# Optimization experiments

Measured on AMD Instinct MI355X. Metric: run time of the kernel, lower is better.

## Reference

```python
import jax, jax.numpy as jnp
import numpy as np

B, S, H, E, V = 64, 512, 1024, 512, 32000
D = 2  # bidirectional encoder -> memory dim = D*H


def setup_inputs() -> dict:
    key = jax.random.key(0)
    ks = jax.random.split(key, 16)
    sc = lambda n: 1.0 / np.sqrt(n)
    return {
        "word": jax.random.randint(ks[0], (B,), 1, V),
        "hidden": jax.random.normal(ks[1], (B, H), jnp.float32),
        "encoder_outputs": jax.random.normal(ks[2], (B, S, D * H), jnp.float32),
        "output_distribution": jax.random.uniform(ks[3], (B, V), jnp.float32),
        "encoder_attention": jax.random.uniform(ks[4], (B, S), jnp.float32),
        # embedding (padding_idx=0 row zeroed)
        "emb": jax.random.normal(ks[5], (V, E), jnp.float32).at[0].set(0.0) * 0.02,
        # Bah_Attn params
        "lin1_w": jax.random.normal(ks[6], (H, H), jnp.float32) * sc(H),
        "lin1_b": jnp.zeros((H,), jnp.float32),
        "lin2_w": jax.random.normal(ks[7], (H, D * H), jnp.float32) * sc(D * H),
        "lin2_b": jnp.zeros((H,), jnp.float32),
        "v_w": jax.random.normal(ks[8], (1, H), jnp.float32) * sc(H),
        "v_b": jnp.zeros((1,), jnp.float32),
        # GRUCell params: input = context(2H) + word_vec(E) = 2560
        "W_ih": jax.random.normal(ks[9], (3 * H, D * H + E), jnp.float32) * sc(H),
        "b_ih": jnp.zeros((3 * H,), jnp.float32),
        "W_hh": jax.random.normal(ks[10], (3 * H, H), jnp.float32) * sc(H),
        "b_hh": jnp.zeros((3 * H,), jnp.float32),
        # output projection
        "out_w": jax.random.normal(ks[11], (V, H), jnp.float32) * sc(H),
        "out_b": jnp.zeros((V,), jnp.float32),
    }


def reference(word, hidden, encoder_outputs, output_distribution, encoder_attention,
              emb, lin1_w, lin1_b, lin2_w, lin2_b, v_w, v_b,
              W_ih, b_ih, W_hh, b_hh, out_w, out_b):
    # word embedding lookup (feed_word_emb='word')
    word_vec = emb[word]                                   # [B, E]
    h_x = hidden @ lin1_w.T + lin1_b                       # [B, H]
    h_m = jnp.einsum('bsm,hm->bsh', encoder_outputs, lin2_w) + lin2_b  # [B, S, H]
    e = jnp.tanh(h_x[:, None, :] + h_m) @ v_w[0] + v_b[0]  # [B, S]
    score = jax.nn.softmax(e, axis=-1)                     # [B, S]
    context = jnp.einsum('bs,bsm->bm', score, encoder_outputs)  # [B, 2H]
    # GRUCell step on cat([context, word_vec])
    x = jnp.concatenate([context, word_vec], axis=1)       # [B, 2H+E]
    gi = x @ W_ih.T + b_ih                                 # [B, 3H]
    gh = hidden @ W_hh.T + b_hh                            # [B, 3H]
    i_r, i_z, i_n = jnp.split(gi, 3, axis=1)
    h_r, h_z, h_n = jnp.split(gh, 3, axis=1)
    r = jax.nn.sigmoid(i_r + h_r)
    z = jax.nn.sigmoid(i_z + h_z)
    n = jnp.tanh(i_n + r * h_n)
    new_hidden = (1.0 - z) * n + z * hidden                # [B, H]
    pred_word = new_hidden @ out_w.T + out_b               # [B, V]
    return (pred_word, new_hidden, score)
```

## Files before the change

kernel.cpp:

```cpp
#include <hip/hip_runtime.h>
#include <hip/hip_bf16.h>
#include <stdint.h>

typedef __attribute__((ext_vector_type(4))) float f32x4;
typedef __attribute__((ext_vector_type(8))) short short8;

#define B_   64
#define S_   512
#define H_   1024
#define E_   512
#define V_   32000
#define M_   2048
#define BS_  32768
#define XIN_ 2560
#define G3_  3072

__device__ __forceinline__ unsigned short f2bf(float f) {
  union { float f; unsigned u; } x; x.f = f;
  unsigned r = x.u + 0x7fffu + ((x.u >> 16) & 1u);
  return (unsigned short)(r >> 16);
}

__device__ __forceinline__ float bf2f(unsigned short u) {
  union { unsigned u; float f; } x; x.u = (unsigned)u << 16; return x.f;
}

__device__ __forceinline__ void async16(const void* g, void* l) {
  __builtin_amdgcn_global_load_lds((const __attribute__((address_space(1))) unsigned*)g,
                                   (__attribute__((address_space(3))) unsigned*)l,
                                   16, 0, 0);
}

__global__ __launch_bounds__(256) void k_conv(const float* __restrict__ enc,
                                              unsigned short* __restrict__ ebf,
                                              const float* __restrict__ lin2w,
                                              unsigned short* __restrict__ bw,
                                              const int* __restrict__ word,
                                              const float* __restrict__ emb,
                                              float* __restrict__ wv) {
  const size_t NENC8 = (size_t)BS_ * M_ / 8;
  const size_t NW8   = (size_t)H_ * M_ / 8;
  const size_t NWV4  = (size_t)B_ * E_ / 4;
  const size_t total = NENC8 + NW8 + NWV4;
  for (size_t idx = (size_t)blockIdx.x * 256 + threadIdx.x; idx < total;
       idx += (size_t)gridDim.x * 256) {
    if (idx < NENC8) {
      f32x4 a = *(const f32x4*)(enc + idx * 8);
      f32x4 b = *(const f32x4*)(enc + idx * 8 + 4);
      short8 o = { (short)f2bf(a.x), (short)f2bf(a.y), (short)f2bf(a.z), (short)f2bf(a.w),
                   (short)f2bf(b.x), (short)f2bf(b.y), (short)f2bf(b.z), (short)f2bf(b.w) };
      *(short8*)(ebf + idx * 8) = o;
    } else if (idx < NENC8 + NW8) {
      size_t i = idx - NENC8;
      f32x4 a = *(const f32x4*)(lin2w + i * 8);
      f32x4 b = *(const f32x4*)(lin2w + i * 8 + 4);
      short8 o = { (short)f2bf(a.x), (short)f2bf(a.y), (short)f2bf(a.z), (short)f2bf(a.w),
                   (short)f2bf(b.x), (short)f2bf(b.y), (short)f2bf(b.z), (short)f2bf(b.w) };
      *(short8*)(bw + i * 8) = o;
    } else {
      size_t i = idx - NENC8 - NW8;
      int i0 = (int)i * 4;
      int b = i0 >> 9, c = i0 & 511;
      f32x4 v = *(const f32x4*)(emb + (size_t)word[b] * E_ + c);
      *(f32x4*)(wv + i0) = v;
    }
  }
}

__global__ __launch_bounds__(256) void k_hx(const float* __restrict__ hidden,
                                            const float* __restrict__ w1,
                                            const float* __restrict__ b1,
                                            const float* __restrict__ b2,
                                            float* __restrict__ hx) {
  __shared__ float hs[64][36];
  __shared__ float Ws[64][36];
  const int t = threadIdx.x;
  const int hbase = blockIdx.x * 64;
  const int hb = t & 15, bb = t >> 4;
  const int srow = t >> 2, sc0 = (t & 3) * 8;
  float acc[4][4] = {};
  for (int kc = 0; kc < H_; kc += 32) {
    *(f32x4*)&hs[srow][sc0]     = *(const f32x4*)(hidden + (size_t)srow * H_ + kc + sc0);
    *(f32x4*)&hs[srow][sc0 + 4] = *(const f32x4*)(hidden + (size_t)srow * H_ + kc + sc0 + 4);
    *(f32x4*)&Ws[srow][sc0]     = *(const f32x4*)(w1 + (size_t)(hbase + srow) * H_ + kc + sc0);
    *(f32x4*)&Ws[srow][sc0 + 4] = *(const f32x4*)(w1 + (size_t)(hbase + srow) * H_ + kc + sc0 + 4);
    __syncthreads();
#pragma unroll
    for (int kk = 0; kk < 32; ++kk) {
      float a[4], w4[4];
#pragma unroll
      for (int i = 0; i < 4; ++i) a[i] = hs[bb * 4 + i][kk];
#pragma unroll
      for (int j = 0; j < 4; ++j) w4[j] = Ws[hb + 16 * j][kk];
#pragma unroll
      for (int i = 0; i < 4; ++i)
#pragma unroll
        for (int j = 0; j < 4; ++j) acc[i][j] += a[i] * w4[j];
    }
    __syncthreads();
  }
#pragma unroll
  for (int i = 0; i < 4; ++i)
#pragma unroll
    for (int j = 0; j < 4; ++j) {
      int h = hbase + hb + 16 * j;
      hx[(size_t)(bb * 4 + i) * H_ + h] = acc[i][j] + b1[h] + b2[h];
    }
}

__global__ __launch_bounds__(512, 4) void k_attn2(const unsigned short* __restrict__ encbf,
                                                  const unsigned short* __restrict__ bw,
                                                  const float* __restrict__ hx,
                                                  const float* __restrict__ vw,
                                                  float* __restrict__ epart) {
  extern __shared__ char smem[];
  const int t = threadIdx.x;
  const int w8 = t >> 6, l = t & 63;
  const int wm = w8 >> 1, wn = w8 & 1;
  const int l15 = l & 15, l4 = l >> 4;
  const int bid = blockIdx.x;
  const int xcd = bid & 7, idx = bid >> 3;
  const int bm = xcd * 16 + (idx >> 3);
  const int bn = idx & 7;
  const int b = bm >> 1;

  f32x4 acc[4][4] = {};

  const unsigned short* Ag = encbf + (size_t)(bm * 256) * M_;
  const unsigned short* Bg = bw + (size_t)(bn * 128) * M_;

  const int lr = l >> 2, lc = l & 3;
  const int sw = (lr >> 1) & 3;
  const unsigned short* aSrc0 = Ag + (size_t)(w8 * 32 + lr) * M_ + (lc ^ sw) * 8;
  const unsigned short* aSrc1 = aSrc0 + (size_t)16 * M_;
  const unsigned short* bSrc  = Bg + (size_t)(w8 * 16 + lr) * M_ + (lc ^ sw) * 8;
  const int slotoff = (l4 ^ ((l15 >> 1) & 3)) * 16;

#define STAGE(buf, kt) do { const int k0 = (kt) * 32;                       \
    char* base_ = smem + (buf) * 24576;                                     \
    async16(aSrc0 + k0, base_ + w8 * 2048 + l * 16);                        \
    async16(aSrc1 + k0, base_ + w8 * 2048 + 1024 + l * 16);                 \
    async16(bSrc  + k0, base_ + 16384 + w8 * 1024 + l * 16); } while (0)

  STAGE(0, 0);
  STAGE(1, 1);
  asm volatile("s_waitcnt vmcnt(3)" ::: "memory");
  __builtin_amdgcn_s_barrier();

  int cur = 0;
  for (int kt = 0; kt < 64; ++kt) {
    int nx2 = cur + 2; if (nx2 >= 3) nx2 -= 3;
    if (kt < 62) STAGE(nx2, kt + 2);
    const char* aBase = smem + cur * 24576;
    const char* bBase = aBase + 16384;
    short8 af[4], bf[4];
#pragma unroll
    for (int m = 0; m < 4; ++m)
      af[m] = *(const short8*)(aBase + (wm * 64 + m * 16 + l15) * 64 + slotoff);
#pragma unroll
    for (int n = 0; n < 4; ++n)
      bf[n] = *(const short8*)(bBase + (wn * 64 + n * 16 + l15) * 64 + slotoff);
    __builtin_amdgcn_s_setprio(1);
#pragma unroll
    for (int m = 0; m < 4; ++m)
#pragma unroll
      for (int n = 0; n < 4; ++n)
        acc[m][n] = __builtin_amdgcn_mfma_f32_16x16x32_bf16(af[m], bf[n], acc[m][n], 0, 0, 0);
    __builtin_amdgcn_s_setprio(0);
    if (kt < 62) {
      asm volatile("s_waitcnt vmcnt(3)" ::: "memory");
    } else {
      asm volatile("s_waitcnt vmcnt(0)" ::: "memory");
    }
    __builtin_amdgcn_s_barrier();
    cur = cur + 1; if (cur >= 3) cur = 0;
  }
#undef STAGE

  const int rbase = bm * 256 + wm * 64;
  const int colbase = bn * 128 + wn * 64;
  const int part = bn * 2 + wn;
#pragma unroll
  for (int m = 0; m < 4; ++m) {
#pragma unroll
    for (int j = 0; j < 4; ++j) {
      int rg = rbase + m * 16 + l4 * 4 + j;
      float sum = 0.f;
#pragma unroll
      for (int n = 0; n < 4; ++n) {
        int h = colbase + n * 16 + l15;
        sum += vw[h] * tanhf(hx[b * H_ + h] + acc[m][n][j]);
      }
      sum += __shfl_xor(sum, 1);
      sum += __shfl_xor(sum, 2);
      sum += __shfl_xor(sum, 4);
      sum += __shfl_xor(sum, 8);
      if (l15 == 0) epart[(size_t)part * BS_ + rg] = sum;
    }
  }
}

__global__ __launch_bounds__(256) void k_attn_bf(const unsigned short* __restrict__ encbf,
                                                 const unsigned short* __restrict__ bw,
                                                 const float* __restrict__ hx,
                                                 const float* __restrict__ vw,
                                                 float* __restrict__ epart) {
  __shared__ unsigned short As[3][4096];
  __shared__ unsigned short Bs[3][4096];
  const int bid = blockIdx.x;
  const int xcd = bid & 7, idx = bid >> 3;
  const int bm = xcd * 32 + (idx >> 3);
  const int bn = idx & 7;
  const int t = threadIdx.x;
  const int l = t & 63, w = t >> 6;
  const int wr = w >> 1, wc = w & 1;
  const int l15 = l & 15, l4 = l >> 4;

  f32x4 acc[4][4] = {};

  const unsigned short* Ag = encbf + (size_t)(bm * 128) * M_;
  const unsigned short* Bg = bw + (size_t)(bn * 128) * M_;

  const int srow = t >> 2;
  const int sc = ((t & 3) ^ ((t >> 3) & 3)) * 8;
  const unsigned short* ApT = Ag + (size_t)srow * M_ + sc;
  const unsigned short* BpT = Bg + (size_t)srow * M_ + sc;
  const int xoff = (l4 ^ ((l15 >> 1) & 3)) * 8;

#define STAGE(buf, kt) do { const int k0 = (kt) * 32;                    \
    async16(ApT + k0,             &As[buf][0]    + (size_t)t * 8);       \
    async16(ApT + 64 * M_ + k0,   &As[buf][2048] + (size_t)t * 8);       \
    async16(BpT + k0,             &Bs[buf][0]    + (size_t)t * 8);       \
    async16(BpT + 64 * M_ + k0,   &Bs[buf][2048] + (size_t)t * 8); } while (0)

  STAGE(0, 0);
  STAGE(1, 1);
  asm volatile("s_waitcnt vmcnt(4)" ::: "memory");
  __builtin_amdgcn_s_barrier();

  int cur = 0;
  for (int kt = 0; kt < 64; ++kt) {
    int nx2 = cur + 2; if (nx2 >= 3) nx2 -= 3;
    if (kt < 62) STAGE(nx2, kt + 2);
    short8 af[4], bf[4];
#pragma unroll
    for (int m = 0; m < 4; ++m)
      af[m] = *(const short8*)(&As[cur][(wr * 64 + m * 16 + l15) * 32 + xoff]);
#pragma unroll
    for (int n = 0; n < 4; ++n)
      bf[n] = *(const short8*)(&Bs[cur][(wc * 64 + n * 16 + l15) * 32 + xoff]);
#pragma unroll
    for (int m = 0; m < 4; ++m)
#pragma unroll
      for (int n = 0; n < 4; ++n)
        acc[m][n] = __builtin_amdgcn_mfma_f32_16x16x32_bf16(af[m], bf[n], acc[m][n], 0, 0, 0);
    if (kt < 62) {
      asm volatile("s_waitcnt vmcnt(4)" ::: "memory");
    } else {
      asm volatile("s_waitcnt vmcnt(0)" ::: "memory");
    }
    __builtin_amdgcn_s_barrier();
    cur = cur + 1; if (cur >= 3) cur = 0;
  }
#undef STAGE

  const int colbase = bn * 128 + wc * 64;
#pragma unroll
  for (int m = 0; m < 4; ++m) {
#pragma unroll
    for (int j = 0; j < 4; ++j) {
      int rloc = wr * 64 + m * 16 + l4 * 4 + j;
      int rg = bm * 128 + rloc;
      int b = rg >> 9;
      float sum = 0.f;
#pragma unroll
      for (int n = 0; n < 4; ++n) {
        int h = colbase + n * 16 + l15;
        sum += vw[h] * tanhf(hx[b * H_ + h] + acc[m][n][j]);
      }
      sum += __shfl_xor(sum, 1);
      sum += __shfl_xor(sum, 2);
      sum += __shfl_xor(sum, 4);
      sum += __shfl_xor(sum, 8);
      if (l15 == 0) epart[(size_t)(bn * 2 + wc) * BS_ + rg] = sum;
    }
  }
}

__global__ __launch_bounds__(256) void k_attn(const float* __restrict__ enc,
                                              const unsigned short* __restrict__ bw,
                                              const float* __restrict__ hx,
                                              const float* __restrict__ vw,
                                              float* __restrict__ epart) {
  __shared__ unsigned short As[128 * 32];
  __shared__ unsigned short Bs[128 * 32];
  const int bid = blockIdx.x;
  const int bm = bid & 255, bn = bid >> 8;
  const int t = threadIdx.x;
  const int l = t & 63, w = t >> 6;
  const int wr = w >> 1, wc = w & 1;
  const int l15 = l & 15, l4 = l >> 4;

  f32x4 acc[4][4] = {};

  const float* Ag = enc + (size_t)(bm * 128) * M_;
  const unsigned short* Bg = bw + (size_t)(bn * 128) * M_;

  const int ar = t >> 3;
  const int ac = (t & 7) * 4;
  const int br = t >> 2;
  const int bc = (t & 3) * 8;

  for (int kt = 0; kt < 64; ++kt) {
    const int k0 = kt * 32;
    async16(Bg + (size_t)br * M_ + k0 + bc, (char*)Bs + (size_t)t * 16);
    async16(Bg + (size_t)(br + 64) * M_ + k0 + bc, (char*)Bs + 4096 + (size_t)t * 16);
#pragma unroll
    for (int j = 0; j < 4; ++j) {
      f32x4 v = *(const f32x4*)(Ag + (size_t)(ar + j * 32) * M_ + k0 + ac);
      ushort4 o = { f2bf(v.x), f2bf(v.y), f2bf(v.z), f2bf(v.w) };
      *(ushort4*)(As + (ar + j * 32) * 32 + ac) = o;
    }
    __syncthreads();
    short8 af[4], bf[4];
#pragma unroll
    for (int m = 0; m < 4; ++m)
      af[m] = *(const short8*)(As + (wr * 64 + m * 16 + l15) * 32 + l4 * 8);
#pragma unroll
    for (int n = 0; n < 4; ++n)
      bf[n] = *(const short8*)(Bs + (wc * 64 + n * 16 + l15) * 32 + l4 * 8);
#pragma unroll
    for (int m = 0; m < 4; ++m)
#pragma unroll
      for (int n = 0; n < 4; ++n)
        acc[m][n] = __builtin_amdgcn_mfma_f32_16x16x32_bf16(af[m], bf[n], acc[m][n], 0, 0, 0);
    __syncthreads();
  }

  const int colbase = bn * 128 + wc * 64;
#pragma unroll
  for (int m = 0; m < 4; ++m) {
#pragma unroll
    for (int j = 0; j < 4; ++j) {
      int rloc = wr * 64 + m * 16 + l4 * 4 + j;
      int rg = bm * 128 + rloc;
      int b = rg >> 9;
      float sum = 0.f;
#pragma unroll
      for (int n = 0; n < 4; ++n) {
        int h = colbase + n * 16 + l15;
        sum += vw[h] * tanhf(hx[b * H_ + h] + acc[m][n][j]);
      }
      sum += __shfl_xor(sum, 1);
      sum += __shfl_xor(sum, 2);
      sum += __shfl_xor(sum, 4);
      sum += __shfl_xor(sum, 8);
      if (l15 == 0) epart[(size_t)(bn * 2 + wc) * BS_ + rg] = sum;
    }
  }
}

__global__ __launch_bounds__(256) void k_softmax(const float* __restrict__ epart,
                                                 float* __restrict__ score) {
  int b = blockIdx.x, t = threadIdx.x;
  float v0 = 0.f, v1 = 0.f;
#pragma unroll
  for (int p = 0; p < 16; ++p) {
    v0 += epart[(size_t)p * BS_ + b * S_ + t];
    v1 += epart[(size_t)p * BS_ + b * S_ + 256 + t];
  }
  int w = t >> 6, l = t & 63;
  float m = fmaxf(v0, v1);
#pragma unroll
  for (int off = 32; off; off >>= 1) m = fmaxf(m, __shfl_xor(m, off));
  __shared__ float sm[4];
  __shared__ float ssum[4];
  if (l == 0) sm[w] = m;
  __syncthreads();
  float M = fmaxf(fmaxf(sm[0], sm[1]), fmaxf(sm[2], sm[3]));
  float p0 = expf(v0 - M), p1 = expf(v1 - M);
  float s = p0 + p1;
#pragma unroll
  for (int off = 32; off; off >>= 1) s += __shfl_xor(s, off);
  if (l == 0) ssum[w] = s;
  __syncthreads();
  float inv = 1.f / (ssum[0] + ssum[1] + ssum[2] + ssum[3]);
  score[b * S_ + t] = p0 * inv;
  score[b * S_ + 256 + t] = p1 * inv;
}

__global__ __launch_bounds__(256) void k_ctxb(const unsigned short* __restrict__ encbf,
                                              const float* __restrict__ score,
                                              float* __restrict__ cpart) {
  int blk = blockIdx.x;
  int b = blk >> 3, sc = blk & 7;
  int t = threadIdx.x;
  int m = t * 8;
  f32x4 acc0 = {0.f, 0.f, 0.f, 0.f}, acc1 = {0.f, 0.f, 0.f, 0.f};
  const unsigned short* ep = encbf + (size_t)(b * S_ + sc * 64) * M_ + m;
  const float* sp = score + b * S_ + sc * 64;
#pragma unroll 4
  for (int s8 = 0; s8 < 64; ++s8) {
    float sv = sp[s8];
    short8 v = *(const short8*)(ep + (size_t)s8 * M_);
    acc0.x += bf2f((unsigned short)v[0]) * sv;
    acc0.y += bf2f((unsigned short)v[1]) * sv;
    acc0.z += bf2f((unsigned short)v[2]) * sv;
    acc0.w += bf2f((unsigned short)v[3]) * sv;
    acc1.x += bf2f((unsigned short)v[4]) * sv;
    acc1.y += bf2f((unsigned short)v[5]) * sv;
    acc1.z += bf2f((unsigned short)v[6]) * sv;
    acc1.w += bf2f((unsigned short)v[7]) * sv;
  }
  float* dst = cpart + (size_t)sc * (B_ * M_) + b * M_ + m;
  *(f32x4*)dst = acc0;
  *(f32x4*)(dst + 4) = acc1;
}

__global__ __launch_bounds__(256) void k_ctx(const float* __restrict__ enc,
                                             const float* __restrict__ score,
                                             float* __restrict__ cpart) {
  int blk = blockIdx.x;
  int b = blk >> 4, mc = (blk >> 3) & 1, sc = blk & 7;
  int t = threadIdx.x;
  int m = mc * 1024 + t * 4;
  f32x4 acc = {0.f, 0.f, 0.f, 0.f};
  const float* ep = enc + (size_t)b * S_ * M_ + m;
  const float* sp = score + b * S_ + sc * 64;
#pragma unroll 4
  for (int s8 = 0; s8 < 64; ++s8) {
    float sv = sp[s8];
    f32x4 v = *(const f32x4*)(ep + (size_t)(sc * 64 + s8) * M_);
    acc += v * sv;
  }
  *(f32x4*)(cpart + (size_t)sc * (B_ * M_) + b * M_ + m) = acc;
}

__global__ void k_ctxred(const float* __restrict__ cpart, float* __restrict__ ctx) {
  int i0 = (blockIdx.x * 256 + threadIdx.x) * 4;
  f32x4 a = {0.f, 0.f, 0.f, 0.f};
#pragma unroll
  for (int p = 0; p < 8; ++p) a += *(const f32x4*)(cpart + (size_t)p * (B_ * M_) + i0);
  *(f32x4*)(ctx + i0) = a;
}

__global__ __launch_bounds__(256) void k_grugemm(const float* __restrict__ ctx,
                                                 const float* __restrict__ wv,
                                                 const float* __restrict__ hidden,
                                                 const float* __restrict__ Wih,
                                                 const float* __restrict__ bih,
                                                 const float* __restrict__ Whh,
                                                 const float* __restrict__ bhh,
                                                 float* __restrict__ gi0,
                                                 float* __restrict__ gi1,
                                                 float* __restrict__ gh0,
                                                 float* __restrict__ gh1) {
  __shared__ float xs[64][36];
  __shared__ float Ws[64][36];
  const int t = threadIdx.x;
  const int blk = blockIdx.x;
  const bool ghh = blk >= 96;
  const int sub = ghh ? blk - 96 : blk;
  const int colt = sub % 48, half = sub / 48;
  const int gbase = colt * 64;
  const int K = ghh ? H_ : XIN_;
  const int klo = ghh ? (half ? 512 : 0) : (half ? 1280 : 0);
  const int khi = ghh ? (half ? 1024 : 512) : (half ? 2560 : 1280);
  const float* Wp = ghh ? Whh : Wih;
  const int vb = t & 15, bb = t >> 4;
  const int srow = t >> 2, sc0 = (t & 3) * 8;
  float acc[4][4] = {};
  for (int kc = klo; kc < khi; kc += 32) {
    f32x4 xa, xb;
    if (ghh) {
      xa = *(const f32x4*)(hidden + (size_t)srow * H_ + kc + sc0);
      xb = *(const f32x4*)(hidden + (size_t)srow * H_ + kc + sc0 + 4);
    } else if (kc + sc0 < M_) {
      xa = *(const f32x4*)(ctx + (size_t)srow * M_ + kc + sc0);
      xb = *(const f32x4*)(ctx + (size_t)srow * M_ + kc + sc0 + 4);
    } else {
      xa = *(const f32x4*)(wv + (size_t)srow * E_ + kc + sc0 - M_);
      xb = *(const f32x4*)(wv + (size_t)srow * E_ + kc + sc0 - M_ + 4);
    }
    *(f32x4*)&xs[srow][sc0] = xa;
    *(f32x4*)&xs[srow][sc0 + 4] = xb;
    *(f32x4*)&Ws[srow][sc0]     = *(const f32x4*)(Wp + (size_t)(gbase + srow) * K + kc + sc0);
    *(f32x4*)&Ws[srow][sc0 + 4] = *(const f32x4*)(Wp + (size_t)(gbase + srow) * K + kc + sc0 + 4);
    __syncthreads();
#pragma unroll
    for (int kk = 0; kk < 32; ++kk) {
      float a[4], w4[4];
#pragma unroll
      for (int i = 0; i < 4; ++i) a[i] = xs[bb * 4 + i][kk];
#pragma unroll
      for (int j = 0; j < 4; ++j) w4[j] = Ws[vb + 16 * j][kk];
#pragma unroll
      for (int i = 0; i < 4; ++i)
#pragma unroll
        for (int j = 0; j < 4; ++j) acc[i][j] += a[i] * w4[j];
    }
    __syncthreads();
  }
  float* dst = ghh ? (half ? gh1 : gh0) : (half ? gi1 : gi0);
  const float* bias = ghh ? bhh : bih;
#pragma unroll
  for (int i = 0; i < 4; ++i)
#pragma unroll
    for (int j = 0; j < 4; ++j) {
      int g = gbase + vb + 16 * j;
      float v = acc[i][j] + (half ? 0.f : bias[g]);
      dst[(size_t)(bb * 4 + i) * G3_ + g] = v;
    }
}

__global__ void k_gate(const float* __restrict__ gi0, const float* __restrict__ gi1,
                       const float* __restrict__ gh0, const float* __restrict__ gh1,
                       const float* __restrict__ hidden, float* __restrict__ newh,
                       unsigned short* __restrict__ newhbf) {
  int o = blockIdx.x * 256 + threadIdx.x;
  int b = o >> 10, h = o & 1023;
  size_t base = (size_t)b * G3_;
  float ir = gi0[base + h] + gi1[base + h];
  float iz = gi0[base + 1024 + h] + gi1[base + 1024 + h];
  float in = gi0[base + 2048 + h] + gi1[base + 2048 + h];
  float hr = gh0[base + h] + gh1[base + h];
  float hz = gh0[base + 1024 + h] + gh1[base + 1024 + h];
  float hn = gh0[base + 2048 + h] + gh1[base + 2048 + h];
  float r = 1.f / (1.f + expf(-(ir + hr)));
  float z = 1.f / (1.f + expf(-(iz + hz)));
  float n = tanhf(in + r * hn);
  float nh = (1.f - z) * n + z * hidden[o];
  newh[o] = nh;
  newhbf[o] = f2bf(nh);
}

__global__ __launch_bounds__(256) void k_outproj_mfma(const unsigned short* __restrict__ newhbf,
                                                      const float* __restrict__ ow,
                                                      const float* __restrict__ ob,
                                                      float* __restrict__ pred) {
  __shared__ unsigned short As[2048];
  __shared__ unsigned short Bs[4096];
  const int t = threadIdx.x;
  const int w = t >> 6, l = t & 63;
  const int l15 = l & 15, l4 = l >> 4;
  const int vbase = blockIdx.x * 128;

  const unsigned short* aSrc = newhbf + (size_t)(t & 63) * H_ + (t >> 6) * 8;
  const int br = t >> 1, bh = t & 1;
  const float* bSrc = ow + (size_t)(vbase + br) * H_ + bh * 16;

  f32x4 acc[4][2] = {};

  for (int kc = 0; kc < H_; kc += 32) {
    async16(aSrc + kc, (char*)As + (size_t)t * 16);
    f32x4 v0 = *(const f32x4*)(bSrc + kc);
    f32x4 v1 = *(const f32x4*)(bSrc + kc + 4);
    f32x4 v2 = *(const f32x4*)(bSrc + kc + 8);
    f32x4 v3 = *(const f32x4*)(bSrc + kc + 12);
    ushort4 p0 = { f2bf(v0.x), f2bf(v0.y), f2bf(v0.z), f2bf(v0.w) };
    ushort4 p1 = { f2bf(v1.x), f2bf(v1.y), f2bf(v1.z), f2bf(v1.w) };
    ushort4 p2 = { f2bf(v2.x), f2bf(v2.y), f2bf(v2.z), f2bf(v2.w) };
    ushort4 p3 = { f2bf(v3.x), f2bf(v3.y), f2bf(v3.z), f2bf(v3.w) };
    const int kg0 = bh * 2;
    *(ushort4*)(Bs + kg0 * 1024 + br * 8)       = p0;
    *(ushort4*)(Bs + kg0 * 1024 + br * 8 + 4)   = p1;
    *(ushort4*)(Bs + (kg0 + 1) * 1024 + br * 8)     = p2;
    *(ushort4*)(Bs + (kg0 + 1) * 1024 + br * 8 + 4) = p3;
    __syncthreads();
    short8 af[4], bf[2];
#pragma unroll
    for (int rf = 0; rf < 4; ++rf)
      af[rf] = *(const short8*)(As + l4 * 512 + (rf * 16 + l15) * 8);
#pragma unroll
    for (int cf = 0; cf < 2; ++cf)
      bf[cf] = *(const short8*)(Bs + l4 * 1024 + (w * 32 + cf * 16 + l15) * 8);
#pragma unroll
    for (int rf = 0; rf < 4; ++rf)
#pragma unroll
      for (int cf = 0; cf < 2; ++cf)
        acc[rf][cf] = __builtin_amdgcn_mfma_f32_16x16x32_bf16(af[rf], bf[cf], acc[rf][cf], 0, 0, 0);
    __syncthreads();
  }

#pragma unroll
  for (int cf = 0; cf < 2; ++cf) {
    int col = vbase + w * 32 + cf * 16 + l15;
    float bias = ob[col];
#pragma unroll
    for (int rf = 0; rf < 4; ++rf)
#pragma unroll
      for (int j = 0; j < 4; ++j) {
        int row = rf * 16 + l4 * 4 + j;
        pred[(size_t)row * V_ + col] = acc[rf][cf][j] + bias;
      }
  }
}

extern "C" void kernel_launch(void* const* d_in, const int* in_sizes, int n_in,
                              void* d_out, int out_size, void* d_ws, size_t ws_size,
                              hipStream_t stream) {
  const int*   word   = (const int*)d_in[0];
  const float* hidden = (const float*)d_in[1];
  const float* enc    = (const float*)d_in[2];
  const float* emb    = (const float*)d_in[5];
  const float* lin1w  = (const float*)d_in[6];
  const float* lin1b  = (const float*)d_in[7];
  const float* lin2w  = (const float*)d_in[8];
  const float* lin2b  = (const float*)d_in[9];
  const float* vw     = (const float*)d_in[10];
  const float* Wih    = (const float*)d_in[12];
  const float* bih    = (const float*)d_in[13];
  const float* Whh    = (const float*)d_in[14];
  const float* bhh    = (const float*)d_in[15];
  const float* ow     = (const float*)d_in[16];
  const float* ob     = (const float*)d_in[17];

  float* out   = (float*)d_out;
  float* pred  = out;
  float* newh  = out + 2048000;
  float* score = out + 2113536;

  const size_t ENCBF = 134217728;
  const bool fast = ws_size >= ENCBF + 13107200;
  char* ws = (char*)d_ws;
  unsigned short* encbf = (unsigned short*)ws;
  size_t base = fast ? ENCBF : 0;
  unsigned short* bw = (unsigned short*)(ws + base);
  float* hx    = (float*)(ws + base + 4194304);
  float* wvbuf = (float*)(ws + base + 4456448);
  float* epart = (float*)(ws + base + 4587520);
  float* cpart = (float*)(ws + base + 6684672);
  float* ctx   = (float*)(ws + base + 10878976);
  float* gi0   = (float*)(ws + base + 11403264);
  float* gh0   = (float*)(ws + base + 12189696);
  unsigned short* nhbf = (unsigned short*)(ws + base + 12976128);
  float* gi1   = epart;
  float* gh1   = epart + 196608;

  bool use2 = false;
  if (fast) {
    hipError_t e = hipFuncSetAttribute((const void*)k_attn2,
        hipFuncAttributeMaxDynamicSharedMemorySize, 73728);
    use2 = (e == hipSuccess);
  }

  k_hx<<<16, 256, 0, stream>>>(hidden, lin1w, lin1b, lin2b, hx);
  if (fast) {
    k_conv<<<4096, 256, 0, stream>>>(enc, encbf, lin2w, bw, word, emb, wvbuf);
    if (use2) {
      k_attn2<<<1024, 512, 73728, stream>>>(encbf, bw, hx, vw, epart);
    } else {
      k_attn_bf<<<2048, 256, 0, stream>>>(encbf, bw, hx, vw, epart);
    }
    k_softmax<<<64, 256, 0, stream>>>(epart, score);
    k_ctxb<<<512, 256, 0, stream>>>(encbf, score, cpart);
  } else {
    k_conv<<<4096, 256, 0, stream>>>(enc, encbf, lin2w, bw, word, emb, wvbuf);
    k_attn<<<2048, 256, 0, stream>>>(enc, bw, hx, vw, epart);
    k_softmax<<<64, 256, 0, stream>>>(epart, score);
    k_ctx<<<1024, 256, 0, stream>>>(enc, score, cpart);
  }
  k_ctxred<<<128, 256, 0, stream>>>(cpart, ctx);
  k_grugemm<<<192, 256, 0, stream>>>(ctx, wvbuf, hidden, Wih, bih, Whh, bhh, gi0, gi1, gh0, gh1);
  k_gate<<<256, 256, 0, stream>>>(gi0, gi1, gh0, gh1, hidden, newh, nhbf);
  k_outproj_mfma<<<250, 256, 0, stream>>>(nhbf, ow, ob, pred);
}
```

Before: 463.1 us.

## Enlarge attention GEMM tile to 256x256 and fuse hx GEMM into conversion kernel

Adds k_attn3, which computes 256x256 output tiles per 512-thread block with 4x8 MFMA fragments per wave and triple-buffered 96KB LDS staging. This halves the number of partial score sums and raises operand reuse per LDS load. The small hidden@lin1 GEMM also moves into extra blocks of the bf16 conversion kernel, saving one launch. The larger tile uses more registers and LDS, leaving only 512 blocks and lower occupancy.

Result: faster. 452.1 us (-2.4%).

```diff
diff --git a/kernel.cpp b/kernel.cpp
--- a/kernel.cpp
+++ b/kernel.cpp
@@ -31,19 +31,61 @@
                                    16, 0, 0);
 }
 
-__global__ __launch_bounds__(256) void k_conv(const float* __restrict__ enc,
-                                              unsigned short* __restrict__ ebf,
-                                              const float* __restrict__ lin2w,
-                                              unsigned short* __restrict__ bw,
-                                              const int* __restrict__ word,
-                                              const float* __restrict__ emb,
-                                              float* __restrict__ wv) {
+__global__ __launch_bounds__(256) void k_convhx(const float* __restrict__ enc,
+                                                unsigned short* __restrict__ ebf,
+                                                const float* __restrict__ lin2w,
+                                                unsigned short* __restrict__ bw,
+                                                const int* __restrict__ word,
+                                                const float* __restrict__ emb,
+                                                float* __restrict__ wv,
+                                                const float* __restrict__ hidden,
+                                                const float* __restrict__ w1,
+                                                const float* __restrict__ b1,
+                                                const float* __restrict__ b2,
+                                                float* __restrict__ hx) {
+  __shared__ float hs[64][36];
+  __shared__ float Ws[64][36];
+  const int t = threadIdx.x;
+  if (blockIdx.x >= 4096) {
+    const int hbase = (blockIdx.x - 4096) * 64;
+    const int hb = t & 15, bb = t >> 4;
+    const int srow = t >> 2, sc0 = (t & 3) * 8;
+    float acc[4][4] = {};
+    for (int kc = 0; kc < H_; kc += 32) {
+      *(f32x4*)&hs[srow][sc0]     = *(const f32x4*)(hidden + (size_t)srow * H_ + kc + sc0);
+      *(f32x4*)&hs[srow][sc0 + 4] = *(const f32x4*)(hidden + (size_t)srow * H_ + kc + sc0 + 4);
+      *(f32x4*)&Ws[srow][sc0]     = *(const f32x4*)(w1 + (size_t)(hbase + srow) * H_ + kc + sc0);
+      *(f32x4*)&Ws[srow][sc0 + 4] = *(const f32x4*)(w1 + (size_t)(hbase + srow) * H_ + kc + sc0 + 4);
+      __syncthreads();
+#pragma unroll
+      for (int kk = 0; kk < 32; ++kk) {
+        float a[4], w4[4];
+#pragma unroll
+        for (int i = 0; i < 4; ++i) a[i] = hs[bb * 4 + i][kk];
+#pragma unroll
+        for (int j = 0; j < 4; ++j) w4[j] = Ws[hb + 16 * j][kk];
+#pragma unroll
+        for (int i = 0; i < 4; ++i)
+#pragma unroll
+          for (int j = 0; j < 4; ++j) acc[i][j] += a[i] * w4[j];
+      }
+      __syncthreads();
+    }
+#pragma unroll
+    for (int i = 0; i < 4; ++i)
+#pragma unroll
+      for (int j = 0; j < 4; ++j) {
+        int h = hbase + hb + 16 * j;
+        hx[(size_t)(bb * 4 + i) * H_ + h] = acc[i][j] + b1[h] + b2[h];
+      }
+    return;
+  }
   const size_t NENC8 = (size_t)BS_ * M_ / 8;
   const size_t NW8   = (size_t)H_ * M_ / 8;
   const size_t NWV4  = (size_t)B_ * E_ / 4;
   const size_t total = NENC8 + NW8 + NWV4;
-  for (size_t idx = (size_t)blockIdx.x * 256 + threadIdx.x; idx < total;
-       idx += (size_t)gridDim.x * 256) {
+  for (size_t idx = (size_t)blockIdx.x * 256 + t; idx < total;
+       idx += (size_t)4096 * 256) {
     if (idx < NENC8) {
       f32x4 a = *(const f32x4*)(enc + idx * 8);
       f32x4 b = *(const f32x4*)(enc + idx * 8 + 4);
@@ -67,45 +109,98 @@
   }
 }
 
-__global__ __launch_bounds__(256) void k_hx(const float* __restrict__ hidden,
-                                            const float* __restrict__ w1,
-                                            const float* __restrict__ b1,
-                                            const float* __restrict__ b2,
-                                            float* __restrict__ hx) {
-  __shared__ float hs[64][36];
-  __shared__ float Ws[64][36];
+__global__ __launch_bounds__(512, 2) void k_attn3(const unsigned short* __restrict__ encbf,
+                                                  const unsigned short* __restrict__ bw,
+                                                  const float* __restrict__ hx,
+                                                  const float* __restrict__ vw,
+                                                  float* __restrict__ epart) {
+  extern __shared__ char smem[];
   const int t = threadIdx.x;
-  const int hbase = blockIdx.x * 64;
-  const int hb = t & 15, bb = t >> 4;
-  const int srow = t >> 2, sc0 = (t & 3) * 8;
-  float acc[4][4] = {};
-  for (int kc = 0; kc < H_; kc += 32) {
-    *(f32x4*)&hs[srow][sc0]     = *(const f32x4*)(hidden + (size_t)srow * H_ + kc + sc0);
-    *(f32x4*)&hs[srow][sc0 + 4] = *(const f32x4*)(hidden + (size_t)srow * H_ + kc + sc0 + 4);
-    *(f32x4*)&Ws[srow][sc0]     = *(const f32x4*)(w1 + (size_t)(hbase + srow) * H_ + kc + sc0);
-    *(f32x4*)&Ws[srow][sc0 + 4] = *(const f32x4*)(w1 + (size_t)(hbase + srow) * H_ + kc + sc0 + 4);
-    __syncthreads();
-#pragma unroll
-    for (int kk = 0; kk < 32; ++kk) {
-      float a[4], w4[4];
-#pragma unroll
-      for (int i = 0; i < 4; ++i) a[i] = hs[bb * 4 + i][kk];
-#pragma unroll
-      for (int j = 0; j < 4; ++j) w4[j] = Ws[hb + 16 * j][kk];
-#pragma unroll
-      for (int i = 0; i < 4; ++i)
-#pragma unroll
-        for (int j = 0; j < 4; ++j) acc[i][j] += a[i] * w4[j];
-    }
-    __syncthreads();
-  }
-#pragma unroll
-  for (int i = 0; i < 4; ++i)
+  const int w8 = t >> 6, l = t & 63;
+  const int wm = w8 >> 1, wn = w8 & 1;
+  const int l15 = l & 15, l4 = l >> 4;
+  const int bid = blockIdx.x;
+  const int xcd = bid & 7, idx = bid >> 3;
+  const int bm = xcd * 16 + (idx >> 2);
+  const int bn = idx & 3;
+  const int b = bm >> 1;
+
+  f32x4 acc[4][8] = {};
+
+  const unsigned short* Ag = encbf + (size_t)(bm * 256) * M_;
+  const unsigned short* Bg = bw + (size_t)(bn * 256) * M_;
+
+  const int lr = l >> 2, lc = l & 3;
+  const int sw = (lr >> 1) & 3;
+  const unsigned short* aSrc0 = Ag + (size_t)(w8 * 32 + lr) * M_ + (lc ^ sw) * 8;
+  const unsigned short* aSrc1 = aSrc0 + (size_t)16 * M_;
+  const unsigned short* bSrc0 = Bg + (size_t)(w8 * 32 + lr) * M_ + (lc ^ sw) * 8;
+  const unsigned short* bSrc1 = bSrc0 + (size_t)16 * M_;
+  const int slotoff = (l4 ^ ((l15 >> 1) & 3)) * 16;
+
+#define STAGE(buf, kt) do { const int k0 = (kt) * 32;                       \
+    char* base_ = smem + (buf) * 32768;                                     \
+    async16(aSrc0 + k0, base_ + w8 * 2048 + l * 16);                        \
+    async16(aSrc1 + k0, base_ + w8 * 2048 + 1024 + l * 16);                 \
+    async16(bSrc0 + k0, base_ + 16384 + w8 * 2048 + l * 16);                \
+    async16(bSrc1 + k0, base_ + 16384 + w8 * 2048 + 1024 + l * 16); } while (0)
+
+  STAGE(0, 0);
+  STAGE(1, 1);
+  asm volatile("s_waitcnt vmcnt(4)" ::: "memory");
+  __builtin_amdgcn_s_barrier();
+
+  int cur = 0;
+  for (int kt = 0; kt < 64; ++kt) {
+    int nx2 = cur + 2; if (nx2 >= 3) nx2 -= 3;
+    if (kt < 62) STAGE(nx2, kt + 2);
+    const char* aBase = smem + cur * 32768;
+    const char* bBase = aBase + 16384;
+    short8 af[4], bf[8];
+#pragma unroll
+    for (int m = 0; m < 4; ++m)
+      af[m] = *(const short8*)(aBase + (wm * 64 + m * 16 + l15) * 64 + slotoff);
+#pragma unroll
+    for (int n = 0; n < 8; ++n)
+      bf[n] = *(const short8*)(bBase + (wn * 128 + n * 16 + l15) * 64 + slotoff);
+    __builtin_amdgcn_s_setprio(1);
+#pragma unroll
+    for (int m = 0; m < 4; ++m)
+#pragma unroll
+      for (int n = 0; n < 8; ++n)
+        acc[m][n] = __builtin_amdgcn_mfma_f32_16x16x32_bf16(af[m], bf[n], acc[m][n], 0, 0, 0);
+    __builtin_amdgcn_s_setprio(0);
+    if (kt < 62) {
+      asm volatile("s_waitcnt vmcnt(4)" ::: "memory");
+    } else {
+      asm volatile("s_waitcnt vmcnt(0)" ::: "memory");
+    }
+    __builtin_amdgcn_s_barrier();
+    cur = cur + 1; if (cur >= 3) cur = 0;
+  }
+#undef STAGE
+
+  const int rbase = bm * 256 + wm * 64;
+  const int colbase = bn * 256 + wn * 128;
+  const int part = bn * 2 + wn;
+#pragma unroll
+  for (int m = 0; m < 4; ++m) {
 #pragma unroll
     for (int j = 0; j < 4; ++j) {
-      int h = hbase + hb + 16 * j;
-      hx[(size_t)(bb * 4 + i) * H_ + h] = acc[i][j] + b1[h] + b2[h];
-    }
+      int rg = rbase + m * 16 + l4 * 4 + j;
+      float sum = 0.f;
+#pragma unroll
+      for (int n = 0; n < 8; ++n) {
+        int h = colbase + n * 16 + l15;
+        sum += vw[h] * tanhf(hx[b * H_ + h] + acc[m][n][j]);
+      }
+      sum += __shfl_xor(sum, 1);
+      sum += __shfl_xor(sum, 2);
+      sum += __shfl_xor(sum, 4);
+      sum += __shfl_xor(sum, 8);
+      if (l15 == 0) epart[(size_t)part * BS_ + rg] = sum;
+    }
+  }
 }
 
 __global__ __launch_bounds__(512, 4) void k_attn2(const unsigned short* __restrict__ encbf,
@@ -200,93 +295,6 @@
   }
 }
 
-__global__ __launch_bounds__(256) void k_attn_bf(const unsigned short* __restrict__ encbf,
-                                                 const unsigned short* __restrict__ bw,
-                                                 const float* __restrict__ hx,
-                                                 const float* __restrict__ vw,
-                                                 float* __restrict__ epart) {
-  __shared__ unsigned short As[3][4096];
-  __shared__ unsigned short Bs[3][4096];
-  const int bid = blockIdx.x;
-  const int xcd = bid & 7, idx = bid >> 3;
-  const int bm = xcd * 32 + (idx >> 3);
-  const int bn = idx & 7;
-  const int t = threadIdx.x;
-  const int l = t & 63, w = t >> 6;
-  const int wr = w >> 1, wc = w & 1;
-  const int l15 = l & 15, l4 = l >> 4;
-
-  f32x4 acc[4][4] = {};
-
-  const unsigned short* Ag = encbf + (size_t)(bm * 128) * M_;
-  const unsigned short* Bg = bw + (size_t)(bn * 128) * M_;
-
-  const int srow = t >> 2;
-  const int sc = ((t & 3) ^ ((t >> 3) & 3)) * 8;
-  const unsigned short* ApT = Ag + (size_t)srow * M_ + sc;
-  const unsigned short* BpT = Bg + (size_t)srow * M_ + sc;
-  const int xoff = (l4 ^ ((l15 >> 1) & 3)) * 8;
-
-#define STAGE(buf, kt) do { const int k0 = (kt) * 32;                    \
-    async16(ApT + k0,             &As[buf][0]    + (size_t)t * 8);       \
-    async16(ApT + 64 * M_ + k0,   &As[buf][2048] + (size_t)t * 8);       \
-    async16(BpT + k0,             &Bs[buf][0]    + (size_t)t * 8);       \
-    async16(BpT + 64 * M_ + k0,   &Bs[buf][2048] + (size_t)t * 8); } while (0)
-
-  STAGE(0, 0);
-  STAGE(1, 1);
-  asm volatile("s_waitcnt vmcnt(4)" ::: "memory");
-  __builtin_amdgcn_s_barrier();
-
-  int cur = 0;
-  for (int kt = 0; kt < 64; ++kt) {
-    int nx2 = cur + 2; if (nx2 >= 3) nx2 -= 3;
-    if (kt < 62) STAGE(nx2, kt + 2);
-    short8 af[4], bf[4];
-#pragma unroll
-    for (int m = 0; m < 4; ++m)
-      af[m] = *(const short8*)(&As[cur][(wr * 64 + m * 16 + l15) * 32 + xoff]);
-#pragma unroll
-    for (int n = 0; n < 4; ++n)
-      bf[n] = *(const short8*)(&Bs[cur][(wc * 64 + n * 16 + l15) * 32 + xoff]);
-#pragma unroll
-    for (int m = 0; m < 4; ++m)
-#pragma unroll
-      for (int n = 0; n < 4; ++n)
-        acc[m][n] = __builtin_amdgcn_mfma_f32_16x16x32_bf16(af[m], bf[n], acc[m][n], 0, 0, 0);
-    if (kt < 62) {
-      asm volatile("s_waitcnt vmcnt(4)" ::: "memory");
-    } else {
-      asm volatile("s_waitcnt vmcnt(0)" ::: "memory");
-    }
-    __builtin_amdgcn_s_barrier();
-    cur = cur + 1; if (cur >= 3) cur = 0;
-  }
-#undef STAGE
-
-  const int colbase = bn * 128 + wc * 64;
-#pragma unroll
-  for (int m = 0; m < 4; ++m) {
-#pragma unroll
-    for (int j = 0; j < 4; ++j) {
-      int rloc = wr * 64 + m * 16 + l4 * 4 + j;
-      int rg = bm * 128 + rloc;
-      int b = rg >> 9;
-      float sum = 0.f;
-#pragma unroll
-      for (int n = 0; n < 4; ++n) {
-        int h = colbase + n * 16 + l15;
-        sum += vw[h] * tanhf(hx[b * H_ + h] + acc[m][n][j]);
-      }
-      sum += __shfl_xor(sum, 1);
-      sum += __shfl_xor(sum, 2);
-      sum += __shfl_xor(sum, 4);
-      sum += __shfl_xor(sum, 8);
-      if (l15 == 0) epart[(size_t)(bn * 2 + wc) * BS_ + rg] = sum;
-    }
-  }
-}
-
 __global__ __launch_bounds__(256) void k_attn(const float* __restrict__ enc,
                                               const unsigned short* __restrict__ bw,
                                               const float* __restrict__ hx,
@@ -361,11 +369,11 @@
 }
 
 __global__ __launch_bounds__(256) void k_softmax(const float* __restrict__ epart,
-                                                 float* __restrict__ score) {
+                                                 float* __restrict__ score,
+                                                 int npart) {
   int b = blockIdx.x, t = threadIdx.x;
   float v0 = 0.f, v1 = 0.f;
-#pragma unroll
-  for (int p = 0; p < 16; ++p) {
+  for (int p = 0; p < npart; ++p) {
     v0 += epart[(size_t)p * BS_ + b * S_ + t];
     v1 += epart[(size_t)p * BS_ + b * S_ + 256 + t];
   }
@@ -637,27 +645,36 @@
   float* gi1   = epart;
   float* gh1   = epart + 196608;
 
-  bool use2 = false;
+  bool use3 = false, use2 = false;
   if (fast) {
-    hipError_t e = hipFuncSetAttribute((const void*)k_attn2,
-        hipFuncAttributeMaxDynamicSharedMemorySize, 73728);
-    use2 = (e == hipSuccess);
-  }
-
-  k_hx<<<16, 256, 0, stream>>>(hidden, lin1w, lin1b, lin2b, hx);
+    use3 = (hipFuncSetAttribute((const void*)k_attn3,
+        hipFuncAttributeMaxDynamicSharedMemorySize, 98304) == hipSuccess);
+    if (!use3)
+      use2 = (hipFuncSetAttribute((const void*)k_attn2,
+          hipFuncAttributeMaxDynamicSharedMemorySize, 73728) == hipSuccess);
+  }
+
   if (fast) {
-    k_conv<<<4096, 256, 0, stream>>>(enc, encbf, lin2w, bw, word, emb, wvbuf);
-    if (use2) {
+    k_convhx<<<4112, 256, 0, stream>>>(enc, encbf, lin2w, bw, word, emb, wvbuf,
+                                       hidden, lin1w, lin1b, lin2b, hx);
+    int npart;
+    if (use3) {
+      k_attn3<<<512, 512, 98304, stream>>>(encbf, bw, hx, vw, epart);
+      npart = 8;
+    } else if (use2) {
       k_attn2<<<1024, 512, 73728, stream>>>(encbf, bw, hx, vw, epart);
+      npart = 16;
     } else {
-      k_attn_bf<<<2048, 256, 0, stream>>>(encbf, bw, hx, vw, epart);
-    }
-    k_softmax<<<64, 256, 0, stream>>>(epart, score);
+      k_attn<<<2048, 256, 0, stream>>>((const float*)d_in[2], bw, hx, vw, epart);
+      npart = 16;
+    }
+    k_softmax<<<64, 256, 0, stream>>>(epart, score, npart);
     k_ctxb<<<512, 256, 0, stream>>>(encbf, score, cpart);
   } else {
-    k_conv<<<4096, 256, 0, stream>>>(enc, encbf, lin2w, bw, word, emb, wvbuf);
+    k_convhx<<<4112, 256, 0, stream>>>(enc, encbf, lin2w, bw, word, emb, wvbuf,
+                                       hidden, lin1w, lin1b, lin2b, hx);
     k_attn<<<2048, 256, 0, stream>>>(enc, bw, hx, vw, epart);
-    k_softmax<<<64, 256, 0, stream>>>(epart, score);
+    k_softmax<<<64, 256, 0, stream>>>(epart, score, 16);
     k_ctx<<<1024, 256, 0, stream>>>(enc, score, cpart);
   }
   k_ctxred<<<128, 256, 0, stream>>>(cpart, ctx);
```
